# Performance work log

Measured on AMD Instinct MI355X. Metric: run time of the kernel, lower is better.

The kernel has to match this reference:

```python
import jax, jax.numpy as jnp
import numpy as np

TRIM_RATIO = 0.1
B, N, D_IN, D_H, N_OUT, D_OUT = 64, 1024, 512, 1024, 10, 1


def setup_inputs() -> dict:
    key = jax.random.key(0)
    ks = jax.random.split(key, 10)
    X = jax.random.normal(ks[0], (B, N, D_IN), dtype=jnp.float32)
    # ragged valid lengths in [N//2, N]; guarantees num_valid > 2*k for trim_ratio=0.1
    lengths = jax.random.randint(ks[1], (B,), N // 2, N + 1)
    mask = (jnp.arange(N)[None, :] < lengths[:, None]).astype(jnp.float32)
    s_in, s_h = 1.0 / np.sqrt(D_IN), 1.0 / np.sqrt(D_H)
    W1 = jax.random.uniform(ks[2], (D_IN, D_H), jnp.float32, -s_in, s_in)
    b1 = jax.random.uniform(ks[3], (D_H,), jnp.float32, -s_in, s_in)
    W2 = jax.random.uniform(ks[4], (D_H, D_H), jnp.float32, -s_h, s_h)
    b2 = jax.random.uniform(ks[5], (D_H,), jnp.float32, -s_h, s_h)
    W3 = jax.random.uniform(ks[6], (D_H, D_H), jnp.float32, -s_h, s_h)
    b3 = jax.random.uniform(ks[7], (D_H,), jnp.float32, -s_h, s_h)
    W4 = jax.random.uniform(ks[8], (D_H, N_OUT * D_OUT), jnp.float32, -s_h, s_h)
    b4 = jax.random.uniform(ks[9], (N_OUT * D_OUT,), jnp.float32, -s_h, s_h)
    return {"X": X, "mask": mask, "W1": W1, "b1": b1, "W2": W2, "b2": b2,
            "W3": W3, "b3": b3, "W4": W4, "b4": b4}


def reference(X, mask, W1, b1, W2, b2, W3, b3, W4, b4):
    # encode MLP: [B,N,D_IN] -> [B,N,D_H]
    encoded = jax.nn.relu(jnp.einsum('bni,ih->bnh', X, W1) + b1) @ W2 + b2
    masked = encoded * mask[..., None]
    num_valid = mask.sum(axis=-1).astype(jnp.int32)                 # [B]
    k = (num_valid.astype(jnp.float32) * TRIM_RATIO).astype(jnp.int32)  # floor, as int()
    # push invalid rows to +inf so valid elements occupy the first num_valid slots after sort
    padded = jnp.where(mask[..., None] > 0, masked, jnp.inf)
    sorted_v = jnp.sort(padded, axis=1)                             # per-column sort, [B,N,D_H]
    pos = jnp.arange(N)[None, :]
    keep = (pos >= k[:, None]) & (pos < (num_valid - k)[:, None])   # [B,N]
    summed = jnp.sum(jnp.where(keep[..., None], sorted_v, 0.0), axis=1)  # [B,D_H]
    denom = (num_valid - 2 * k).astype(jnp.float32)[:, None]
    aggregated = summed / denom                                     # trimmed mean
    # decode MLP
    out = jax.nn.relu(aggregated @ W3 + b3) @ W4 + b4               # [B, N_OUT*D_OUT]
    out = out.reshape(-1, N_OUT, D_OUT).squeeze(-1)                 # [B, N_OUT]
    return out
```

## Files before the change

kernel.cpp:

```cpp
#include <hip/hip_runtime.h>


typedef _Float16 half8  __attribute__((ext_vector_type(8)));
typedef _Float16 half4v __attribute__((ext_vector_type(4)));
typedef float    floatx4 __attribute__((ext_vector_type(4)));

#define GLD_LDS(g, l)                                                                     \
  __builtin_amdgcn_global_load_lds((const __attribute__((address_space(1))) void*)(g),    \
                                   (__attribute__((address_space(3))) void*)(l), 16, 0, 0)

__global__ void prep_nv(const float* __restrict__ mask, int* __restrict__ nv_arr,
                        int* __restrict__ k_arr) {
  int b = blockIdx.x, lane = threadIdx.x;
  const float4* mp = (const float4*)(mask + (b << 10));
  float s = 0.f;
#pragma unroll
  for (int i = 0; i < 4; ++i) {
    float4 v = mp[lane + i * 64];
    s += v.x + v.y + v.z + v.w;
  }
#pragma unroll
  for (int off = 32; off > 0; off >>= 1) s += __shfl_xor(s, off, 64);
  if (lane == 0) {
    int nv = (int)(s + 0.5f);
    int kk = (int)((float)nv * 0.1f);
    nv_arr[b] = nv;
    k_arr[b] = kk;
  }
}

__device__ __forceinline__ void transpose_body(const float* __restrict__ W,
                                               _Float16* __restrict__ WT, int R, int C,
                                               int r0, int c0, _Float16 (*tile)[65]) {
  for (int i = threadIdx.x; i < 4096; i += 256) {
    int r = i >> 6, c = i & 63;
    tile[r][c] = (_Float16)W[(size_t)(r0 + r) * C + c0 + c];
  }
  __syncthreads();
  for (int i = threadIdx.x; i < 4096; i += 256) {
    int c = i >> 6, r = i & 63;
    WT[(size_t)(c0 + c) * R + r0 + r] = tile[r][c];
  }
}

__global__ __launch_bounds__(256) void preprocess(
    const float* __restrict__ X, _Float16* __restrict__ X16,
    const float* __restrict__ W1, _Float16* __restrict__ W1T,
    const float* __restrict__ W2, _Float16* __restrict__ W2T,
    const int* __restrict__ nv_arr) {
  __shared__ _Float16 tile[64][65];
  int bid = blockIdx.x;
  if (bid < 16384) {
    int n0 = (bid << 2) & 1023;
    int batch = bid >> 8;
    int nv = nv_arr[batch];
    if (n0 >= ((nv + 127) & ~127)) return;
    int i = (bid * 256 + threadIdx.x) * 8;
    float4 a = *(const float4*)(X + i);
    float4 c = *(const float4*)(X + i + 4);
    half8 h;
    h[0] = (_Float16)a.x; h[1] = (_Float16)a.y; h[2] = (_Float16)a.z; h[3] = (_Float16)a.w;
    h[4] = (_Float16)c.x; h[5] = (_Float16)c.y; h[6] = (_Float16)c.z; h[7] = (_Float16)c.w;
    *(half8*)(X16 + i) = h;
  } else if (bid < 16384 + 128) {
    int id = bid - 16384;
    transpose_body(W1, W1T, 512, 1024, (id & 7) * 64, (id >> 3) * 64, tile);
  } else {
    int id = bid - 16512;
    transpose_body(W2, W2T, 1024, 1024, (id & 15) * 64, (id >> 4) * 64, tile);
  }
}

template <int KDIM, int MODE>
__global__ __launch_bounds__(256, 3) void gemm_kernel_sm(
    const _Float16* __restrict__ Aop, const _Float16* __restrict__ Bop,
    const float* __restrict__ bias, const int* __restrict__ nv_arr,
    _Float16* __restrict__ outp) {
  __shared__ __align__(16) _Float16 ldsA[128 * 64];
  __shared__ __align__(16) _Float16 ldsB[128 * 64];
  int i0, j0;
  int bid = blockIdx.x;
  int fat = (((bid >> 6) << 3) | (bid & 7)) * 128;
  int thin = ((bid >> 3) & 7) * 128;
  if (MODE == 1) {
    i0 = thin; j0 = fat;
    if ((j0 & 1023) >= nv_arr[j0 >> 10]) return;
  } else {
    i0 = fat; j0 = thin;
    if ((i0 & 1023) >= nv_arr[i0 >> 10]) return;
  }
  const int t = threadIdx.x, lane = t & 63;
  const int wv = t >> 6, wi = wv & 1, wj = wv >> 1;
  const int lr = lane & 15, q = lane >> 4;

  floatx4 acc[4][4] = {};

  const int gch = (t & 7) ^ ((t >> 3) & 7);
  const _Float16* gA[4];
  const _Float16* gB[4];
  _Float16* lA[4];
  _Float16* lB[4];
#pragma unroll
  for (int r = 0; r < 4; ++r) {
    int row = r * 32 + (t >> 3);
    gA[r] = Aop + (size_t)(i0 + row) * KDIM + gch * 8;
    gB[r] = Bop + (size_t)(j0 + row) * KDIM + gch * 8;
    lA[r] = ldsA + (r * 256 + (t & ~63)) * 8;
    lB[r] = ldsB + (r * 256 + (t & ~63)) * 8;
  }

  int aoff[4], boff[4];
#pragma unroll
  for (int mi = 0; mi < 4; ++mi) {
    int row = wi * 64 + mi * 16 + lr;
    aoff[mi] = row * 64 + ((q ^ (row & 7)) * 8);
  }
#pragma unroll
  for (int nj = 0; nj < 4; ++nj) {
    int row = wj * 64 + nj * 16 + lr;
    boff[nj] = row * 64 + ((q ^ (row & 7)) * 8);
  }

  for (int kt = 0; kt < KDIM / 64; ++kt) {
#pragma unroll
    for (int r = 0; r < 4; ++r) GLD_LDS(gA[r], lA[r]);
#pragma unroll
    for (int r = 0; r < 4; ++r) GLD_LDS(gB[r], lB[r]);
#pragma unroll
    for (int r = 0; r < 4; ++r) { gA[r] += 64; gB[r] += 64; }
    __syncthreads();
#pragma unroll
    for (int kk = 0; kk < 2; ++kk) {
      half8 af[4], bf[4];
#pragma unroll
      for (int mi = 0; mi < 4; ++mi) af[mi] = *(const half8*)&ldsA[aoff[mi] ^ (kk * 32)];
#pragma unroll
      for (int nj = 0; nj < 4; ++nj) bf[nj] = *(const half8*)&ldsB[boff[nj] ^ (kk * 32)];
#pragma unroll
      for (int mi = 0; mi < 4; ++mi)
#pragma unroll
        for (int nj = 0; nj < 4; ++nj)
          acc[mi][nj] =
              __builtin_amdgcn_mfma_f32_16x16x32_f16(af[mi], bf[nj], acc[mi][nj], 0, 0, 0);
    }
    __syncthreads();
  }

  if (MODE == 1) {
#pragma unroll
    for (int mi = 0; mi < 4; ++mi) {
      int ih = i0 + wi * 64 + mi * 16 + q * 4;
      floatx4 bb = *(const floatx4*)&bias[ih];
#pragma unroll
      for (int nj = 0; nj < 4; ++nj) {
        int j = j0 + wj * 64 + nj * 16 + lr;
        floatx4 v = acc[mi][nj];
        half4v hv;
#pragma unroll
        for (int r = 0; r < 4; ++r) hv[r] = (_Float16)fmaxf(v[r] + bb[r], 0.f);
        *(half4v*)&outp[(size_t)j * 1024 + ih] = hv;
      }
    }
  } else {
#pragma unroll
    for (int nj = 0; nj < 4; ++nj) {
      int j = j0 + wj * 64 + nj * 16 + lr;
      float bj = bias[j];
#pragma unroll
      for (int mi = 0; mi < 4; ++mi) {
        int im = i0 + wi * 64 + mi * 16 + q * 4;
        int bb = im >> 10, n = im & 1023;
        floatx4 v = acc[mi][nj];
        half4v hv;
#pragma unroll
        for (int r = 0; r < 4; ++r) hv[r] = (_Float16)(v[r] + bj);
        *(half4v*)&outp[((size_t)bb << 20) + ((size_t)j << 10) + (size_t)n] = hv;
      }
    }
  }
}

template <int KDIM, int MODE>
__global__ __launch_bounds__(512, 2) void gemm_kernel(
    const _Float16* __restrict__ Aop, const _Float16* __restrict__ Bop,
    const float* __restrict__ bias, const int* __restrict__ nv_arr,
    _Float16* __restrict__ outp) {
  constexpr int NT = KDIM / 64;
  __shared__ __align__(16) _Float16 lds[2][2][256 * 64];

  int bid = blockIdx.x;
  int fat = ((((bid >> 5) << 3) | (bid & 7))) << 8;
  int thin = ((bid >> 3) & 3) << 8;
  int i0, j0;
  if (MODE == 1) {
    i0 = thin; j0 = fat;
    if ((j0 & 1023) >= nv_arr[j0 >> 10]) return;
  } else {
    i0 = fat; j0 = thin;
    if ((i0 & 1023) >= nv_arr[i0 >> 10]) return;
  }
  const int t = threadIdx.x, lane = t & 63;
  const int wv = t >> 6, wm = wv & 1, wn = wv >> 1;
  const int lr = lane & 15, q = lane >> 4;
  const int swz = (q ^ (lr & 7)) * 8;

  const int gch = (t & 7) ^ ((t >> 3) & 7);
  const _Float16* gA = Aop + (size_t)(i0 + (t >> 3)) * KDIM + gch * 8;
  const _Float16* gB = Bop + (size_t)(j0 + (t >> 3)) * KDIM + gch * 8;

#define STG(OP, BUF, KT, R)                                                   \
  GLD_LDS(((OP) ? gB : gA) + (size_t)(R) * 64 * KDIM + (size_t)(KT) * 64,     \
          &lds[BUF][OP][((R) * 512 + (t & ~63)) * 8])

  floatx4 acc[8][4] = {};
  half8 af[4][2];
  half8 bf[2][2][2];

#define LD_A(BUF, IH)                                                         \
  _Pragma("unroll") for (int f = 0; f < 4; ++f)                               \
  _Pragma("unroll") for (int kk = 0; kk < 2; ++kk)                            \
      af[f][kk] = *(const half8*)&lds[BUF][0]                                 \
          [(((wm << 7) + ((IH) << 6) + (f << 4) + lr) << 6) + (swz ^ (kk << 5))];

#define LD_B_HALF(BUF, JH)                                                    \
  _Pragma("unroll") for (int g = 0; g < 2; ++g)                               \
  _Pragma("unroll") for (int kk = 0; kk < 2; ++kk)                            \
      bf[JH][g][kk] = *(const half8*)&lds[BUF][1]                             \
          [(((wn << 6) + ((JH) << 5) + (g << 4) + lr) << 6) + (swz ^ (kk << 5))];

#define MFMA_QUAD(IH, JH)                                                     \
  __builtin_amdgcn_s_setprio(1);                                              \
  _Pragma("unroll") for (int f = 0; f < 4; ++f)                               \
  _Pragma("unroll") for (int g = 0; g < 2; ++g)                               \
  _Pragma("unroll") for (int kk = 0; kk < 2; ++kk)                            \
      acc[((IH) << 2) + f][((JH) << 1) + g] =                                 \
          __builtin_amdgcn_mfma_f32_16x16x32_f16(                             \
              af[f][kk], bf[JH][g][kk], acc[((IH) << 2) + f][((JH) << 1) + g], 0, 0, 0); \
  __builtin_amdgcn_s_setprio(0);

#define TILE(KT, CUR, DO_STG, DO_B1)                                          \
  {                                                                           \
    LD_A(CUR, 0);                                                             \
    LD_B_HALF(CUR, 0);                                                        \
    LD_B_HALF(CUR, 1);                                                        \
    MFMA_QUAD(0, 0);                                                          \
    MFMA_QUAD(0, 1);                                                          \
    LD_A(CUR, 1);                                                             \
    asm volatile("s_waitcnt lgkmcnt(0)" ::: "memory");                        \
    __builtin_amdgcn_sched_barrier(0);                                        \
    __builtin_amdgcn_s_barrier();            \
    __builtin_amdgcn_sched_barrier(0);                                        \
    if (DO_STG) { STG(0, CUR, (KT) + 2, 0); STG(0, CUR, (KT) + 2, 1);         \
                  STG(1, CUR, (KT) + 2, 0); STG(1, CUR, (KT) + 2, 1);         \
                  STG(0, CUR, (KT) + 2, 2); STG(0, CUR, (KT) + 2, 3);         \
                  STG(1, CUR, (KT) + 2, 2); STG(1, CUR, (KT) + 2, 3); }       \
    MFMA_QUAD(1, 0);                                                          \
    MFMA_QUAD(1, 1);                                                          \
    if (DO_B1) {                                                              \
      if (DO_STG) { asm volatile("s_waitcnt vmcnt(8)" ::: "memory"); }        \
      else        { asm volatile("s_waitcnt vmcnt(0)" ::: "memory"); }        \
      __builtin_amdgcn_sched_barrier(0);                                      \
      __builtin_amdgcn_s_barrier();                 \
      __builtin_amdgcn_sched_barrier(0);                                      \
    }                                                                         \
  }

  STG(0, 0, 0, 0); STG(0, 0, 0, 1); STG(0, 0, 0, 2); STG(0, 0, 0, 3);
  STG(1, 0, 0, 0); STG(1, 0, 0, 1); STG(1, 0, 0, 2); STG(1, 0, 0, 3);
  STG(0, 1, 1, 0); STG(0, 1, 1, 1); STG(0, 1, 1, 2); STG(0, 1, 1, 3);
  STG(1, 1, 1, 0); STG(1, 1, 1, 1); STG(1, 1, 1, 2); STG(1, 1, 1, 3);
  asm volatile("s_waitcnt vmcnt(8)" ::: "memory");
  __builtin_amdgcn_s_barrier();
  __builtin_amdgcn_sched_barrier(0);

  for (int kt = 0; kt < NT - 2; kt += 2) {
    TILE(kt, 0, 1, 1);
    TILE(kt + 1, 1, 1, 1);
  }
  TILE(NT - 2, 0, 0, 1);
  TILE(NT - 1, 1, 0, 0);

  if (MODE == 1) {
#pragma unroll
    for (int mi = 0; mi < 8; ++mi) {
      int ih = i0 + (wm << 7) + (mi << 4) + (q << 2);
      floatx4 bb = *(const floatx4*)&bias[ih];
#pragma unroll
      for (int nj = 0; nj < 4; ++nj) {
        int j = j0 + (wn << 6) + (nj << 4) + lr;
        floatx4 v = acc[mi][nj];
        half4v hv;
#pragma unroll
        for (int r = 0; r < 4; ++r) hv[r] = (_Float16)fmaxf(v[r] + bb[r], 0.f);
        *(half4v*)&outp[(size_t)j * 1024 + ih] = hv;
      }
    }
  } else {
#pragma unroll
    for (int nj = 0; nj < 4; ++nj) {
      int j = j0 + (wn << 6) + (nj << 4) + lr;
      float bj = bias[j];
#pragma unroll
      for (int mi = 0; mi < 8; ++mi) {
        int im = i0 + (wm << 7) + (mi << 4) + (q << 2);
        int bb = im >> 10, n = im & 1023;
        floatx4 v = acc[mi][nj];
        half4v hv;
#pragma unroll
        for (int r = 0; r < 4; ++r) hv[r] = (_Float16)(v[r] + bj);
        *(half4v*)&outp[((size_t)bb << 20) + ((size_t)j << 10) + (size_t)n] = hv;
      }
    }
  }
}

#define NB 1024
__global__ __launch_bounds__(256) void trim_kernel(const _Float16* __restrict__ encT,
                                                   const int* __restrict__ nv_arr,
                                                   const int* __restrict__ k_arr,
                                                   float* __restrict__ agg) {
  __shared__ unsigned int cnt[4 * NB];
  int t = threadIdx.x, lane = t & 63, w = t >> 6;
  int blk = blockIdx.x;
  int batch = blk >> 8;
  int h = ((blk & 255) << 2) + w;
  unsigned int* cw = cnt + w * NB;
  uint4* cp = (uint4*)cw;
  {
    uint4 z = {0u, 0u, 0u, 0u};
#pragma unroll
    for (int i = 0; i < 4; ++i) cp[lane * 4 + (i ^ ((lane >> 1) & 3))] = z;
  }

  int nv = nv_arr[batch], kk = k_arr[batch];
  const _Float16* col = encT + ((size_t)batch << 20) + ((size_t)h << 10);
  const uint4* p = (const uint4*)col + lane * 2;
  uint4 u0 = p[0], u1 = p[1];
  unsigned vals[8] = {u0.x, u0.y, u0.z, u0.w, u1.x, u1.y, u1.z, u1.w};
  int nvalid = nv - lane * 16;

  float vv[16];
  int bn[16];
#pragma unroll
  for (int d = 0; d < 8; ++d) {
    unsigned u = vals[d];
#pragma unroll
    for (int sub = 0; sub < 2; ++sub) {
      int idx = d * 2 + sub;
      unsigned short bits = (unsigned short)(sub ? (u >> 16) : (u & 0xffffu));
      _Float16 hvv;
      __builtin_memcpy(&hvv, &bits, 2);
      float v = (float)hvv;
      if (idx < nvalid) {
        v = fminf(fmaxf(v, -8.0f), 7.999f);
        int bin = (int)((v + 8.0f) * 64.0f);
        bin = min(NB - 1, bin);
        vv[idx] = v;
        bn[idx] = bin;
        int Lb = bin >> 4, jc = (bin >> 2) & 3;
        int phys = ((Lb << 2) + (jc ^ ((Lb >> 1) & 3))) * 4 + (bin & 3);
        atomicAdd(&cw[phys], 1u);
      } else {
        vv[idx] = 0.f;
        bn[idx] = -1;
      }
    }
  }

  int c[16];
  {
    uint4 rb[4];
#pragma unroll
    for (int i = 0; i < 4; ++i) rb[i] = cp[lane * 4 + (i ^ ((lane >> 1) & 3))];
#pragma unroll
    for (int i = 0; i < 4; ++i) {
      c[4 * i] = (int)rb[i].x; c[4 * i + 1] = (int)rb[i].y;
      c[4 * i + 2] = (int)rb[i].z; c[4 * i + 3] = (int)rb[i].w;
    }
  }
  int ct = 0;
#pragma unroll
  for (int i = 0; i < 16; ++i) ct += c[i];
  int ci = ct;
#pragma unroll
  for (int off = 1; off < 64; off <<= 1) {
    int cu = __shfl_up(ci, off, 64);
    if (lane >= off) ci += cu;
  }
  int cex = ci - ct;
  int r1 = kk, r2 = nv - kk;
  int p1 = -1, p2 = -1;
  {
    int run = cex;
#pragma unroll
    for (int i = 0; i < 16; ++i) {
      int cc = c[i];
      if (run < r1 && r1 <= run + cc) p1 = ((lane * 16 + i) << 12) | run;
      if (run < r2 && r2 <= run + cc) p2 = ((lane * 16 + i) << 12) | run;
      run += cc;
    }
  }
#pragma unroll
  for (int off = 32; off > 0; off >>= 1) {
    p1 = max(p1, __shfl_xor(p1, off, 64));
    p2 = max(p2, __shfl_xor(p2, off, 64));
  }
  int b1 = p1 >> 12, cex1 = p1 & 4095;
  int b2 = p2 >> 12, cex2 = p2 & 4095;
  float s1 = 0.f, s2 = 0.f, tm = 0.f;
  int c1 = 0, c2 = 0;
#pragma unroll
  for (int i = 0; i < 16; ++i) {
    int b = bn[i];
    float v = vv[i];
    if (b == b1) { s1 += v; c1++; }
    if (b == b2) { s2 += v; c2++; }
    if (b > b1 && b < b2) tm += v;
  }
#pragma unroll
  for (int off = 32; off > 0; off >>= 1) {
    s1 += __shfl_xor(s1, off, 64);
    s2 += __shfl_xor(s2, off, 64);
    tm += __shfl_xor(tm, off, 64);
    c1 += __shfl_xor(c1, off, 64);
    c2 += __shfl_xor(c2, off, 64);
  }
  float mid;
  if (b1 == b2) {
    mid = (float)(r2 - r1) * (s1 / (float)c1);
  } else {
    mid = (float)(cex1 + c1 - r1) * (s1 / (float)c1) + tm +
          (float)(r2 - cex2) * (s2 / (float)c2);
  }
  if (lane == 0) {
    agg[(batch << 10) + h] = mid / (float)(nv - 2 * kk);
  }
}

__global__ __launch_bounds__(256) void decode1(const float* __restrict__ agg,
                                               const float* __restrict__ W3,
                                               const float* __restrict__ b3,
                                               float* __restrict__ A3) {
  __shared__ float al[1024];
  __shared__ float red[256];
  int b = blockIdx.x, hb = blockIdx.y, t = threadIdx.x;
  for (int i = t; i < 1024; i += 256) al[i] = agg[(b << 10) + i];
  __syncthreads();
  int hl = t & 63, ks = t >> 6;
  int h = hb * 64 + hl;
  const float* wp = W3 + (size_t)(ks * 256) * 1024 + h;
  const float* ap = al + ks * 256;
  float acc = 0.f;
#pragma unroll 8
  for (int k = 0; k < 256; ++k) acc = fmaf(ap[k], wp[(size_t)k * 1024], acc);
  red[t] = acc;
  __syncthreads();
  if (t < 64) {
    float s = red[t] + red[t + 64] + red[t + 128] + red[t + 192] + b3[hb * 64 + t];
    A3[(b << 10) + hb * 64 + t] = fmaxf(s, 0.f);
  }
}

__global__ void decode2(const float* __restrict__ A3, const float* __restrict__ W4,
                        const float* __restrict__ b4, float* __restrict__ outp) {
  __shared__ float red[4][10];
  int b = blockIdx.x, t = threadIdx.x, lane = t & 63, w = t >> 6;
  float part[10];
#pragma unroll
  for (int o = 0; o < 10; ++o) part[o] = 0.f;
#pragma unroll
  for (int jj = 0; jj < 4; ++jj) {
    int h2 = jj * 256 + t;
    float a = A3[(b << 10) + h2];
#pragma unroll
    for (int o = 0; o < 10; ++o) part[o] = fmaf(a, W4[h2 * 10 + o], part[o]);
  }
#pragma unroll
  for (int o = 0; o < 10; ++o)
#pragma unroll
    for (int off = 32; off > 0; off >>= 1) part[o] += __shfl_xor(part[o], off, 64);
  if (lane == 0)
#pragma unroll
    for (int o = 0; o < 10; ++o) red[w][o] = part[o];
  __syncthreads();
  if (t < 10) outp[b * 10 + t] = b4[t] + red[0][t] + red[1][t] + red[2][t] + red[3][t];
}

extern "C" void kernel_launch(void* const* d_in, const int* in_sizes, int n_in,
                              void* d_out, int out_size, void* d_ws, size_t ws_size,
                              hipStream_t stream) {
  const float* X = (const float*)d_in[0];
  const float* mask = (const float*)d_in[1];
  const float* W1 = (const float*)d_in[2];
  const float* b1 = (const float*)d_in[3];
  const float* W2 = (const float*)d_in[4];
  const float* b2 = (const float*)d_in[5];
  const float* W3 = (const float*)d_in[6];
  const float* b3 = (const float*)d_in[7];
  const float* W4 = (const float*)d_in[8];
  const float* b4 = (const float*)d_in[9];
  float* outp = (float*)d_out;
  char* ws = (char*)d_ws;

  _Float16* X16 = (_Float16*)(ws);
  _Float16* H1 = (_Float16*)(ws + 67108864ull);
  _Float16* encT = (_Float16*)(ws + 201326592ull);
  _Float16* W1T = (_Float16*)(ws + 335544320ull);
  _Float16* W2T = (_Float16*)(ws + 336592896ull);
  float* agg = (float*)(ws + 338690048ull);
  float* A3 = (float*)(ws + 338952192ull);
  int* nv_arr = (int*)(ws + 339214336ull);
  int* k_arr = (int*)(ws + 339214592ull);

  prep_nv<<<64, 64, 0, stream>>>(mask, nv_arr, k_arr);
  preprocess<<<16768, 256, 0, stream>>>(X, X16, W1, W1T, W2, W2T, nv_arr);
  gemm_kernel_sm<512, 1><<<4096, 256, 0, stream>>>(W1T, X16, b1, nv_arr, H1);
  gemm_kernel<1024, 2><<<1024, 512, 0, stream>>>(H1, W2T, b2, nv_arr, encT);
  trim_kernel<<<16384, 256, 0, stream>>>(encT, nv_arr, k_arr, agg);
  decode1<<<dim3(64, 16), 256, 0, stream>>>(agg, W3, b3, A3);
  decode2<<<64, 256, 0, stream>>>(A3, W4, b4, outp);
}
```

Baseline: 527.7 us.

## Fuse fp32-to-fp16 conversion of X into first GEMM's LDS load path

Removes the separate pass that converted X to fp16 in a workspace buffer. The first GEMM now loads fp32 X tiles straight into LDS with a swizzled layout and converts them to fp16 while forming MFMA operands. This drops one full write and re-read of X16. In exchange the B tile takes twice the LDS, which may reduce occupancy, and each inner step does extra conversion work. The trim kernel also skips global loads for column chunks beyond the valid length.

```diff
diff --git a/kernel.cpp b/kernel.cpp
--- a/kernel.cpp
+++ b/kernel.cpp
@@ -44,90 +44,63 @@
 }
 
 __global__ __launch_bounds__(256) void preprocess(
-    const float* __restrict__ X, _Float16* __restrict__ X16,
     const float* __restrict__ W1, _Float16* __restrict__ W1T,
-    const float* __restrict__ W2, _Float16* __restrict__ W2T,
-    const int* __restrict__ nv_arr) {
+    const float* __restrict__ W2, _Float16* __restrict__ W2T) {
   __shared__ _Float16 tile[64][65];
   int bid = blockIdx.x;
-  if (bid < 16384) {
-    int n0 = (bid << 2) & 1023;
-    int batch = bid >> 8;
-    int nv = nv_arr[batch];
-    if (n0 >= ((nv + 127) & ~127)) return;
-    int i = (bid * 256 + threadIdx.x) * 8;
-    float4 a = *(const float4*)(X + i);
-    float4 c = *(const float4*)(X + i + 4);
-    half8 h;
-    h[0] = (_Float16)a.x; h[1] = (_Float16)a.y; h[2] = (_Float16)a.z; h[3] = (_Float16)a.w;
-    h[4] = (_Float16)c.x; h[5] = (_Float16)c.y; h[6] = (_Float16)c.z; h[7] = (_Float16)c.w;
-    *(half8*)(X16 + i) = h;
-  } else if (bid < 16384 + 128) {
-    int id = bid - 16384;
-    transpose_body(W1, W1T, 512, 1024, (id & 7) * 64, (id >> 3) * 64, tile);
+  if (bid < 128) {
+    transpose_body(W1, W1T, 512, 1024, (bid & 7) * 64, (bid >> 3) * 64, tile);
   } else {
-    int id = bid - 16512;
+    int id = bid - 128;
     transpose_body(W2, W2T, 1024, 1024, (id & 15) * 64, (id >> 4) * 64, tile);
   }
 }
 
-template <int KDIM, int MODE>
-__global__ __launch_bounds__(256, 3) void gemm_kernel_sm(
-    const _Float16* __restrict__ Aop, const _Float16* __restrict__ Bop,
+__global__ __launch_bounds__(256, 3) void gemm1_fused(
+    const _Float16* __restrict__ W1T, const float* __restrict__ X,
     const float* __restrict__ bias, const int* __restrict__ nv_arr,
     _Float16* __restrict__ outp) {
   __shared__ __align__(16) _Float16 ldsA[128 * 64];
-  __shared__ __align__(16) _Float16 ldsB[128 * 64];
-  int i0, j0;
+  __shared__ __align__(16) float ldsB[128 * 64];
   int bid = blockIdx.x;
-  int fat = (((bid >> 6) << 3) | (bid & 7)) * 128;
-  int thin = ((bid >> 3) & 7) * 128;
-  if (MODE == 1) {
-    i0 = thin; j0 = fat;
-    if ((j0 & 1023) >= nv_arr[j0 >> 10]) return;
-  } else {
-    i0 = fat; j0 = thin;
-    if ((i0 & 1023) >= nv_arr[i0 >> 10]) return;
-  }
+  int j0 = (((bid >> 6) << 3) | (bid & 7)) * 128;
+  int i0 = ((bid >> 3) & 7) * 128;
+  if ((j0 & 1023) >= nv_arr[j0 >> 10]) return;
   const int t = threadIdx.x, lane = t & 63;
   const int wv = t >> 6, wi = wv & 1, wj = wv >> 1;
   const int lr = lane & 15, q = lane >> 4;
 
   floatx4 acc[4][4] = {};
 
-  const int gch = (t & 7) ^ ((t >> 3) & 7);
+  const int gchA = (t & 7) ^ ((t >> 3) & 7);
   const _Float16* gA[4];
-  const _Float16* gB[4];
   _Float16* lA[4];
-  _Float16* lB[4];
 #pragma unroll
   for (int r = 0; r < 4; ++r) {
-    int row = r * 32 + (t >> 3);
-    gA[r] = Aop + (size_t)(i0 + row) * KDIM + gch * 8;
-    gB[r] = Bop + (size_t)(j0 + row) * KDIM + gch * 8;
+    gA[r] = W1T + (size_t)(i0 + r * 32 + (t >> 3)) * 512 + gchA * 8;
     lA[r] = ldsA + (r * 256 + (t & ~63)) * 8;
-    lB[r] = ldsB + (r * 256 + (t & ~63)) * 8;
-  }
-
-  int aoff[4], boff[4];
+  }
+  const int gchB = (t & 15) ^ ((t >> 4) & 15);
+  const float* gB = X + (size_t)(j0 + (t >> 4)) * 512 + gchB * 4;
+  float* lB = ldsB + (t & ~63) * 4;
+
+  int aoff[4], brow[4];
 #pragma unroll
   for (int mi = 0; mi < 4; ++mi) {
     int row = wi * 64 + mi * 16 + lr;
     aoff[mi] = row * 64 + ((q ^ (row & 7)) * 8);
   }
 #pragma unroll
-  for (int nj = 0; nj < 4; ++nj) {
-    int row = wj * 64 + nj * 16 + lr;
-    boff[nj] = row * 64 + ((q ^ (row & 7)) * 8);
-  }
-
-  for (int kt = 0; kt < KDIM / 64; ++kt) {
+  for (int nj = 0; nj < 4; ++nj) brow[nj] = wj * 64 + nj * 16 + lr;
+
+  for (int kt = 0; kt < 8; ++kt) {
 #pragma unroll
     for (int r = 0; r < 4; ++r) GLD_LDS(gA[r], lA[r]);
 #pragma unroll
-    for (int r = 0; r < 4; ++r) GLD_LDS(gB[r], lB[r]);
-#pragma unroll
-    for (int r = 0; r < 4; ++r) { gA[r] += 64; gB[r] += 64; }
+    for (int R = 0; R < 8; ++R)
+      GLD_LDS(gB + (size_t)R * 16 * 512 + kt * 64, lB + R * 1024);
+#pragma unroll
+    for (int r = 0; r < 4; ++r) gA[r] += 64;
     __syncthreads();
 #pragma unroll
     for (int kk = 0; kk < 2; ++kk) {
@@ -135,7 +108,18 @@
 #pragma unroll
       for (int mi = 0; mi < 4; ++mi) af[mi] = *(const half8*)&ldsA[aoff[mi] ^ (kk * 32)];
 #pragma unroll
-      for (int nj = 0; nj < 4; ++nj) bf[nj] = *(const half8*)&ldsB[boff[nj] ^ (kk * 32)];
+      for (int nj = 0; nj < 4; ++nj) {
+        int rb = brow[nj];
+        int c0 = kk * 8 + q * 2;
+        floatx4 f0 = *(const floatx4*)&ldsB[rb * 64 + ((c0 ^ (rb & 15)) << 2)];
+        floatx4 f1 = *(const floatx4*)&ldsB[rb * 64 + (((c0 + 1) ^ (rb & 15)) << 2)];
+        half8 h;
+        h[0] = (_Float16)f0.x; h[1] = (_Float16)f0.y;
+        h[2] = (_Float16)f0.z; h[3] = (_Float16)f0.w;
+        h[4] = (_Float16)f1.x; h[5] = (_Float16)f1.y;
+        h[6] = (_Float16)f1.z; h[7] = (_Float16)f1.w;
+        bf[nj] = h;
+      }
 #pragma unroll
       for (int mi = 0; mi < 4; ++mi)
 #pragma unroll
@@ -146,36 +130,18 @@
     __syncthreads();
   }
 
-  if (MODE == 1) {
-#pragma unroll
-    for (int mi = 0; mi < 4; ++mi) {
-      int ih = i0 + wi * 64 + mi * 16 + q * 4;
-      floatx4 bb = *(const floatx4*)&bias[ih];
-#pragma unroll
-      for (int nj = 0; nj < 4; ++nj) {
-        int j = j0 + wj * 64 + nj * 16 + lr;
-        floatx4 v = acc[mi][nj];
-        half4v hv;
-#pragma unroll
-        for (int r = 0; r < 4; ++r) hv[r] = (_Float16)fmaxf(v[r] + bb[r], 0.f);
-        *(half4v*)&outp[(size_t)j * 1024 + ih] = hv;
-      }
-    }
-  } else {
+#pragma unroll
+  for (int mi = 0; mi < 4; ++mi) {
+    int ih = i0 + wi * 64 + mi * 16 + q * 4;
+    floatx4 bb = *(const floatx4*)&bias[ih];
 #pragma unroll
     for (int nj = 0; nj < 4; ++nj) {
       int j = j0 + wj * 64 + nj * 16 + lr;
-      float bj = bias[j];
-#pragma unroll
-      for (int mi = 0; mi < 4; ++mi) {
-        int im = i0 + wi * 64 + mi * 16 + q * 4;
-        int bb = im >> 10, n = im & 1023;
-        floatx4 v = acc[mi][nj];
-        half4v hv;
-#pragma unroll
-        for (int r = 0; r < 4; ++r) hv[r] = (_Float16)(v[r] + bj);
-        *(half4v*)&outp[((size_t)bb << 20) + ((size_t)j << 10) + (size_t)n] = hv;
-      }
+      floatx4 v = acc[mi][nj];
+      half4v hv;
+#pragma unroll
+      for (int r = 0; r < 4; ++r) hv[r] = (_Float16)fmaxf(v[r] + bb[r], 0.f);
+      *(half4v*)&outp[(size_t)j * 1024 + ih] = hv;
     }
   }
 }
@@ -333,11 +299,13 @@
   }
 
   int nv = nv_arr[batch], kk = k_arr[batch];
+  int nvalid = nv - lane * 16;
   const _Float16* col = encT + ((size_t)batch << 20) + ((size_t)h << 10);
   const uint4* p = (const uint4*)col + lane * 2;
-  uint4 u0 = p[0], u1 = p[1];
+  uint4 z4 = {0u, 0u, 0u, 0u};
+  uint4 u0 = (nvalid > 0) ? p[0] : z4;
+  uint4 u1 = (nvalid > 8) ? p[1] : z4;
   unsigned vals[8] = {u0.x, u0.y, u0.z, u0.w, u1.x, u1.y, u1.z, u1.w};
-  int nvalid = nv - lane * 16;
 
   float vv[16];
   int bn[16];
@@ -502,7 +470,6 @@
   float* outp = (float*)d_out;
   char* ws = (char*)d_ws;
 
-  _Float16* X16 = (_Float16*)(ws);
   _Float16* H1 = (_Float16*)(ws + 67108864ull);
   _Float16* encT = (_Float16*)(ws + 201326592ull);
   _Float16* W1T = (_Float16*)(ws + 335544320ull);
@@ -513,8 +480,8 @@
   int* k_arr = (int*)(ws + 339214592ull);
 
   prep_nv<<<64, 64, 0, stream>>>(mask, nv_arr, k_arr);
-  preprocess<<<16768, 256, 0, stream>>>(X, X16, W1, W1T, W2, W2T, nv_arr);
-  gemm_kernel_sm<512, 1><<<4096, 256, 0, stream>>>(W1T, X16, b1, nv_arr, H1);
+  preprocess<<<384, 256, 0, stream>>>(W1, W1T, W2, W2T);
+  gemm1_fused<<<4096, 256, 0, stream>>>(W1T, X, b1, nv_arr, H1);
   gemm_kernel<1024, 2><<<1024, 512, 0, stream>>>(H1, W2T, b2, nv_arr, encT);
   trim_kernel<<<16384, 256, 0, stream>>>(encT, nv_arr, k_arr, agg);
   decode1<<<dim3(64, 16), 256, 0, stream>>>(agg, W3, b3, A3);
```

New measurement: 522.7 us. About the same (-1.0%).
